# Performance work log

Hardware: AMD Instinct MI355X
Metric: run time of the kernel (lower is better)

## Reference

```python
import jax, jax.numpy as jnp
import numpy as np

N_ROWS = 4096   # output features (N)
M_COLS = 4096   # input features (M)
BATCH = 4096
NNZ_PER_ROW = 819


def setup_inputs() -> dict:
    rng = np.random.default_rng(0)
    # sample NNZ_PER_ROW distinct, sorted column indices per row (CSR structure)
    cols = np.argsort(rng.random((N_ROWS, M_COLS)), axis=1)[:, :NNZ_PER_ROW]
    cols = np.sort(cols, axis=1).reshape(-1).astype(np.int32)            # [nnz]
    row_ids = np.repeat(np.arange(N_ROWS, dtype=np.int32), NNZ_PER_ROW)  # [nnz], expanded indptr

    key = jax.random.key(0)
    k1, k2, k3 = jax.random.split(key, 3)
    inp = jax.random.normal(k1, (BATCH, M_COLS), dtype=jnp.float32)
    W_val = jax.random.normal(k2, (N_ROWS * NNZ_PER_ROW,), dtype=jnp.float32) * 0.02
    bias = jax.random.normal(k3, (N_ROWS,), dtype=jnp.float32)
    return {
        "input": inp,
        "W_val": W_val,
        "bias": bias,
        "row_ids": jnp.asarray(row_ids),
        "cols": jnp.asarray(cols),
        "N": N_ROWS,
    }


def reference(input, W_val, bias, row_ids, cols, N):
    # Faithful math of SparseLinearFunction: y = x @ W^T + bias where W is the
    # CSR matrix (W_val, row_ids, cols) of shape (N, M). Densify via scatter
    # (CSR has unique (row, col) pairs) then use a single GEMM.
    M = input.shape[-1]
    W = jnp.zeros((N, M), dtype=W_val.dtype).at[row_ids, cols].set(W_val)  # [N, M]
    return jnp.matmul(input, W.T) + bias  # [B, N]
```

## Files before the change

### kernel.cpp

```cpp
#include <hip/hip_runtime.h>
#include <hip/hip_bf16.h>
#include <stdint.h>


#define B_DIM 4096
#define M_DIM 4096
#define N_DIM 4096
#define NNZ_ROW 819

typedef __attribute__((ext_vector_type(8))) __bf16 bf16x8;
typedef __attribute__((ext_vector_type(4))) float f32x4;

__device__ __forceinline__ unsigned short f32_to_bf16(float f) {
    union { float f; unsigned int u; } v;
    v.f = f;
    unsigned int r = v.u + 0x7FFFu + ((v.u >> 16) & 1u);
    return (unsigned short)(r >> 16);
}

__device__ __forceinline__ void load_lds16(const void* g, void* l) {
    __builtin_amdgcn_global_load_lds(
        (const __attribute__((address_space(1))) void*)g,
        (__attribute__((address_space(3))) void*)l,
        16, 0, 0);
}

__global__ __launch_bounds__(256) void prep(
    const float* __restrict__ wval,
    const int* __restrict__ cols,
    unsigned short* __restrict__ wb,
    const float4* __restrict__ x,
    uint4* __restrict__ xb) {
    const int tid = threadIdx.x;
    if (blockIdx.x >= N_DIM) {
        const int i = (blockIdx.x - N_DIM) * 256 + tid;
        const float4 a = x[2 * i];
        const float4 b = x[2 * i + 1];
        union { ushort ush[8]; uint4 u4; } o;
        o.ush[0] = f32_to_bf16(a.x); o.ush[1] = f32_to_bf16(a.y);
        o.ush[2] = f32_to_bf16(a.z); o.ush[3] = f32_to_bf16(a.w);
        o.ush[4] = f32_to_bf16(b.x); o.ush[5] = f32_to_bf16(b.y);
        o.ush[6] = f32_to_bf16(b.z); o.ush[7] = f32_to_bf16(b.w);
        xb[i] = o.u4;
        return;
    }
    __shared__ __attribute__((aligned(16))) unsigned short row_s[M_DIM];
    const int row = blockIdx.x;
    uint4* rs4 = (uint4*)row_s;
    rs4[tid]       = make_uint4(0u, 0u, 0u, 0u);
    rs4[tid + 256] = make_uint4(0u, 0u, 0u, 0u);
    __syncthreads();
    const size_t base = (size_t)row * NNZ_ROW;
    for (int j = tid; j < NNZ_ROW; j += 256) {
        const int c = cols[base + j];
        row_s[c] = f32_to_bf16(wval[base + j]);
    }
    __syncthreads();
    uint4* dst = (uint4*)(wb + (size_t)row * M_DIM);
    dst[tid]       = rs4[tid];
    dst[tid + 256] = rs4[tid + 256];
}

__device__ __forceinline__ void stage_half(
    const unsigned short* __restrict__ src,
    int grow0, int kt, unsigned short* dst, int w, int l) {
#pragma unroll
    for (int j = 0; j < 2; ++j) {
        const int seg = w * 2 + j;
        const int r   = seg * 8 + (l >> 3);
        const int cg  = (l >> 3) ^ (l & 7);
        load_lds16(src + (size_t)(grow0 + r) * M_DIM + kt + cg * 8,
                   dst + seg * 512);
    }
}

template <int MA, int KS, bool RDB, int SK, int WAITN>
__device__ __forceinline__ void phase_op(
    const unsigned short* As_c, const unsigned short* Bs_c,
    unsigned short* As_n, unsigned short* Bs_n,
    const unsigned short* __restrict__ Xb, const unsigned short* __restrict__ Wb,
    int bm0, int bn0, int kn, bool do_stage,
    int wr, int wc, int w, int l,
    bf16x8 (&bfr)[2][2], f32x4 (&acc)[2][4][2][2]) {
    const int l15 = l & 15;
    const int lg  = l >> 4;
    const int lx  = l & 7;
    const int ck  = ((KS * 4 + lg) ^ lx) << 3;

    const unsigned short* Ab = As_c + (MA * 128 + wr * 64 + l15) * 64;
    bf16x8 af[4];
#pragma unroll
    for (int mf = 0; mf < 4; ++mf)
        af[mf] = *(const bf16x8*)(Ab + mf * 1024 + ck);

    if constexpr (RDB) {
#pragma unroll
        for (int nb = 0; nb < 2; ++nb) {
            const unsigned short* Bb = Bs_c + (nb * 128 + wc * 32 + l15) * 64;
#pragma unroll
            for (int nf = 0; nf < 2; ++nf)
                bfr[nb][nf] = *(const bf16x8*)(Bb + nf * 1024 + ck);
        }
    }

    if (do_stage) {
        if constexpr (SK == 0) {
            stage_half(Xb, bm0,       kn, As_n,        w, l);
            stage_half(Wb, bn0,       kn, Bs_n,        w, l);
        }
        if constexpr (SK == 1) stage_half(Wb, bn0 + 128, kn, Bs_n + 8192, w, l);
        if constexpr (SK == 2) stage_half(Xb, bm0 + 128, kn, As_n + 8192, w, l);
    }

    if constexpr (WAITN >= 0) __builtin_amdgcn_s_waitcnt(0x0F70 | WAITN);
    __builtin_amdgcn_s_barrier();

    __builtin_amdgcn_s_setprio(1);
#pragma unroll
    for (int mf = 0; mf < 4; ++mf)
#pragma unroll
        for (int nb = 0; nb < 2; ++nb)
#pragma unroll
            for (int nf = 0; nf < 2; ++nf)
                acc[MA][mf][nb][nf] = __builtin_amdgcn_mfma_f32_16x16x32_bf16(
                    af[mf], bfr[nb][nf], acc[MA][mf][nb][nf], 0, 0, 0);
    __builtin_amdgcn_s_setprio(0);
    __builtin_amdgcn_s_barrier();
    __builtin_amdgcn_sched_barrier(0);
}

__global__ __launch_bounds__(512, 2) void gemm_bt_bias(
    const unsigned short* __restrict__ Xb,
    const unsigned short* __restrict__ Wb,
    const float* __restrict__ bias,
    float* __restrict__ out)
{
    __shared__ __attribute__((aligned(16))) unsigned short As0[16384];
    __shared__ __attribute__((aligned(16))) unsigned short Bs0[16384];
    __shared__ __attribute__((aligned(16))) unsigned short As1[16384];
    __shared__ __attribute__((aligned(16))) unsigned short Bs1[16384];

    const int tid = threadIdx.x;
    const int w   = tid >> 6;
    const int l   = tid & 63;
    const int wr  = w >> 2;
    const int wc  = w & 3;

    const int wg  = blockIdx.y * 16 + blockIdx.x;
    const int idx = ((wg & 7) << 5) | (wg >> 3);
    const int bm0 = (idx >> 4) * 256;
    const int bn0 = (idx & 15) * 256;

    f32x4 acc[2][4][2][2];
#pragma unroll
    for (int a = 0; a < 2; ++a)
#pragma unroll
        for (int b = 0; b < 4; ++b)
#pragma unroll
            for (int c = 0; c < 2; ++c)
#pragma unroll
                for (int d = 0; d < 2; ++d) acc[a][b][c][d] = (f32x4)0.0f;

    bf16x8 bfr[2][2];

    stage_half(Xb, bm0,       0, As0,        w, l);
    stage_half(Wb, bn0,       0, Bs0,        w, l);
    stage_half(Xb, bm0 + 128, 0, As0 + 8192, w, l);
    stage_half(Wb, bn0 + 128, 0, Bs0 + 8192, w, l);
    __builtin_amdgcn_s_waitcnt(0x0F70);
    __builtin_amdgcn_s_barrier();

#define TILE4(AC, BC, AN, BN, KN, DS)                                          \
    phase_op<0, 0, true , 0,  4>(AC, BC, AN, BN, Xb, Wb, bm0, bn0, KN, DS,     \
                                 wr, wc, w, l, bfr, acc);                      \
    phase_op<1, 0, false, 1, -1>(AC, BC, AN, BN, Xb, Wb, bm0, bn0, KN, DS,     \
                                 wr, wc, w, l, bfr, acc);                      \
    phase_op<0, 1, true , 2, -1>(AC, BC, AN, BN, Xb, Wb, bm0, bn0, KN, DS,     \
                                 wr, wc, w, l, bfr, acc);                      \
    phase_op<1, 1, false, 3,  2>(AC, BC, AN, BN, Xb, Wb, bm0, bn0, KN, DS,     \
                                 wr, wc, w, l, bfr, acc);

#pragma unroll 1
    for (int kt = 0; kt < M_DIM - 128; kt += 128) {
        const int k1 = kt + 64;
        const int k2 = kt + 128;
        TILE4(As0, Bs0, As1, Bs1, k1, true)
        TILE4(As1, Bs1, As0, Bs0, k2, true)
    }
    TILE4(As0, Bs0, As1, Bs1, M_DIM - 64, true)
    phase_op<0, 0, true , 3,  0>(As1, Bs1, As0, Bs0, Xb, Wb, bm0, bn0, 0, false,
                                 wr, wc, w, l, bfr, acc);
    phase_op<1, 0, false, 3, -1>(As1, Bs1, As0, Bs0, Xb, Wb, bm0, bn0, 0, false,
                                 wr, wc, w, l, bfr, acc);
    phase_op<0, 1, true , 3, -1>(As1, Bs1, As0, Bs0, Xb, Wb, bm0, bn0, 0, false,
                                 wr, wc, w, l, bfr, acc);
    phase_op<1, 1, false, 3, -1>(As1, Bs1, As0, Bs0, Xb, Wb, bm0, bn0, 0, false,
                                 wr, wc, w, l, bfr, acc);
#undef TILE4

    const int l15 = l & 15;
    const int lg  = l >> 4;
#pragma unroll
    for (int nb = 0; nb < 2; ++nb)
#pragma unroll
        for (int nf = 0; nf < 2; ++nf) {
            const int col = bn0 + nb * 128 + wc * 32 + nf * 16 + l15;
            const float bv = bias[col];
#pragma unroll
            for (int ma = 0; ma < 2; ++ma)
#pragma unroll
                for (int mf = 0; mf < 4; ++mf) {
                    const int row0 = bm0 + ma * 128 + wr * 64 + mf * 16 + lg * 4;
#pragma unroll
                    for (int r = 0; r < 4; ++r)
                        out[(size_t)(row0 + r) * N_DIM + col] =
                            acc[ma][mf][nb][nf][r] + bv;
                }
        }
}


extern "C" void kernel_launch(void* const* d_in, const int* in_sizes, int n_in,
                              void* d_out, int out_size, void* d_ws, size_t ws_size,
                              hipStream_t stream) {
    const float* x       = (const float*)d_in[0];
    const float* wval    = (const float*)d_in[1];
    const float* bias    = (const float*)d_in[2];
    const int*   cols    = (const int*)d_in[4];
    float* out = (float*)d_out;

    unsigned short* Wb = (unsigned short*)d_ws;
    unsigned short* Xb = Wb + (size_t)N_DIM * M_DIM;

    prep<<<dim3(N_DIM + (B_DIM * M_DIM) / 8 / 256), dim3(256), 0, stream>>>(
        wval, cols, Wb, (const float4*)x, (uint4*)Xb);
    gemm_bt_bias<<<dim3(N_DIM / 256, B_DIM / 256), dim3(512), 0, stream>>>(
        Xb, Wb, bias, out);
}
```

Before: 280.1 us.

## Restructure GEMM k-loop into one barrier per k-tile with interleaved LDS reads

The four-phase-per-k-tile schedule is replaced by a single ktile routine. It waits for all outstanding global-to-LDS loads and hits one barrier per tile, then issues all four half-tile stages for the next buffer at once. LDS fragment reads for the next MFMA group are interleaved between the MFMA groups, removing the per-phase double barriers and the staggered partial waitcnts. This cuts synchronization overhead but uses more fragment registers and drops the finer-grained overlap of staging with compute.

```diff
diff --git a/kernel.cpp b/kernel.cpp
--- a/kernel.cpp
+++ b/kernel.cpp
@@ -74,59 +74,79 @@
     }
 }
 
-template <int MA, int KS, bool RDB, int SK, int WAITN>
-__device__ __forceinline__ void phase_op(
+#define MFMA_STEP(MA, ASET, BSET)                                              \
+    __builtin_amdgcn_s_setprio(1);                                             \
+    _Pragma("unroll")                                                          \
+    for (int mf = 0; mf < 4; ++mf)                                             \
+        _Pragma("unroll")                                                      \
+        for (int nb = 0; nb < 2; ++nb)                                         \
+            _Pragma("unroll")                                                  \
+            for (int nf = 0; nf < 2; ++nf)                                     \
+                acc[MA][mf][nb][nf] =                                          \
+                    __builtin_amdgcn_mfma_f32_16x16x32_bf16(                   \
+                        ASET[mf], BSET[nb][nf], acc[MA][mf][nb][nf], 0, 0, 0); \
+    __builtin_amdgcn_s_setprio(0);
+
+__device__ __forceinline__ void ktile(
     const unsigned short* As_c, const unsigned short* Bs_c,
     unsigned short* As_n, unsigned short* Bs_n,
     const unsigned short* __restrict__ Xb, const unsigned short* __restrict__ Wb,
-    int bm0, int bn0, int kn, bool do_stage,
-    int wr, int wc, int w, int l,
-    bf16x8 (&bfr)[2][2], f32x4 (&acc)[2][4][2][2]) {
+    int bm0, int bn0, int knext, bool do_stage,
+    int wr, int wc, int w, int l, f32x4 (&acc)[2][4][2][2])
+{
+    __builtin_amdgcn_s_waitcnt(0x0F70);
+    __builtin_amdgcn_s_barrier();
+
     const int l15 = l & 15;
     const int lg  = l >> 4;
     const int lx  = l & 7;
-    const int ck  = ((KS * 4 + lg) ^ lx) << 3;
-
-    const unsigned short* Ab = As_c + (MA * 128 + wr * 64 + l15) * 64;
-    bf16x8 af[4];
-#pragma unroll
-    for (int mf = 0; mf < 4; ++mf)
-        af[mf] = *(const bf16x8*)(Ab + mf * 1024 + ck);
-
-    if constexpr (RDB) {
-#pragma unroll
-        for (int nb = 0; nb < 2; ++nb) {
-            const unsigned short* Bb = Bs_c + (nb * 128 + wc * 32 + l15) * 64;
-#pragma unroll
-            for (int nf = 0; nf < 2; ++nf)
-                bfr[nb][nf] = *(const bf16x8*)(Bb + nf * 1024 + ck);
-        }
-    }
-
+    const int ck0 = (lg ^ lx) << 3;
+    const int ck1 = ((4 + lg) ^ lx) << 3;
+
+    const unsigned short* A0 = As_c + (wr * 64 + l15) * 64;
+    const unsigned short* A1 = A0 + 128 * 64;
+    const unsigned short* B0 = Bs_c + (wc * 32 + l15) * 64;
+    const unsigned short* B1 = B0 + 128 * 64;
+
+    bf16x8 a0k0[4], a1k0[4], a0k1[4], a1k1[4], bk0[2][2], bk1[2][2];
+
+#pragma unroll
+    for (int mf = 0; mf < 4; ++mf)
+        a0k0[mf] = *(const bf16x8*)(A0 + mf * 1024 + ck0);
+#pragma unroll
+    for (int nf = 0; nf < 2; ++nf) {
+        bk0[0][nf] = *(const bf16x8*)(B0 + nf * 1024 + ck0);
+        bk0[1][nf] = *(const bf16x8*)(B1 + nf * 1024 + ck0);
+    }
     if (do_stage) {
-        if constexpr (SK == 0) {
-            stage_half(Xb, bm0,       kn, As_n,        w, l);
-            stage_half(Wb, bn0,       kn, Bs_n,        w, l);
-        }
-        if constexpr (SK == 1) stage_half(Wb, bn0 + 128, kn, Bs_n + 8192, w, l);
-        if constexpr (SK == 2) stage_half(Xb, bm0 + 128, kn, As_n + 8192, w, l);
-    }
-
-    if constexpr (WAITN >= 0) __builtin_amdgcn_s_waitcnt(0x0F70 | WAITN);
-    __builtin_amdgcn_s_barrier();
-
-    __builtin_amdgcn_s_setprio(1);
-#pragma unroll
-    for (int mf = 0; mf < 4; ++mf)
-#pragma unroll
-        for (int nb = 0; nb < 2; ++nb)
-#pragma unroll
-            for (int nf = 0; nf < 2; ++nf)
-                acc[MA][mf][nb][nf] = __builtin_amdgcn_mfma_f32_16x16x32_bf16(
-                    af[mf], bfr[nb][nf], acc[MA][mf][nb][nf], 0, 0, 0);
-    __builtin_amdgcn_s_setprio(0);
-    __builtin_amdgcn_s_barrier();
-    __builtin_amdgcn_sched_barrier(0);
+        stage_half(Xb, bm0,       knext, As_n,        w, l);
+        stage_half(Wb, bn0,       knext, Bs_n,        w, l);
+        stage_half(Xb, bm0 + 128, knext, As_n + 8192, w, l);
+        stage_half(Wb, bn0 + 128, knext, Bs_n + 8192, w, l);
+    }
+#pragma unroll
+    for (int mf = 0; mf < 4; ++mf)
+        a1k0[mf] = *(const bf16x8*)(A1 + mf * 1024 + ck0);
+
+    MFMA_STEP(0, a0k0, bk0)
+
+#pragma unroll
+    for (int mf = 0; mf < 4; ++mf)
+        a0k1[mf] = *(const bf16x8*)(A0 + mf * 1024 + ck1);
+#pragma unroll
+    for (int nf = 0; nf < 2; ++nf) {
+        bk1[0][nf] = *(const bf16x8*)(B0 + nf * 1024 + ck1);
+        bk1[1][nf] = *(const bf16x8*)(B1 + nf * 1024 + ck1);
+    }
+
+    MFMA_STEP(1, a1k0, bk0)
+
+#pragma unroll
+    for (int mf = 0; mf < 4; ++mf)
+        a1k1[mf] = *(const bf16x8*)(A1 + mf * 1024 + ck1);
+
+    MFMA_STEP(0, a0k1, bk1)
+    MFMA_STEP(1, a1k1, bk1)
 }
 
 __global__ __launch_bounds__(512, 2) void gemm_bt_bias(
@@ -161,42 +181,18 @@
 #pragma unroll
                 for (int d = 0; d < 2; ++d) acc[a][b][c][d] = (f32x4)0.0f;
 
-    bf16x8 bfr[2][2];
-
     stage_half(Xb, bm0,       0, As0,        w, l);
     stage_half(Wb, bn0,       0, Bs0,        w, l);
     stage_half(Xb, bm0 + 128, 0, As0 + 8192, w, l);
     stage_half(Wb, bn0 + 128, 0, Bs0 + 8192, w, l);
-    __builtin_amdgcn_s_waitcnt(0x0F70);
-    __builtin_amdgcn_s_barrier();
-
-#define TILE4(AC, BC, AN, BN, KN, DS)                                          \
-    phase_op<0, 0, true , 0,  4>(AC, BC, AN, BN, Xb, Wb, bm0, bn0, KN, DS,     \
-                                 wr, wc, w, l, bfr, acc);                      \
-    phase_op<1, 0, false, 1, -1>(AC, BC, AN, BN, Xb, Wb, bm0, bn0, KN, DS,     \
-                                 wr, wc, w, l, bfr, acc);                      \
-    phase_op<0, 1, true , 2, -1>(AC, BC, AN, BN, Xb, Wb, bm0, bn0, KN, DS,     \
-                                 wr, wc, w, l, bfr, acc);                      \
-    phase_op<1, 1, false, 3,  2>(AC, BC, AN, BN, Xb, Wb, bm0, bn0, KN, DS,     \
-                                 wr, wc, w, l, bfr, acc);
 
 #pragma unroll 1
-    for (int kt = 0; kt < M_DIM - 128; kt += 128) {
-        const int k1 = kt + 64;
-        const int k2 = kt + 128;
-        TILE4(As0, Bs0, As1, Bs1, k1, true)
-        TILE4(As1, Bs1, As0, Bs0, k2, true)
-    }
-    TILE4(As0, Bs0, As1, Bs1, M_DIM - 64, true)
-    phase_op<0, 0, true , 3,  0>(As1, Bs1, As0, Bs0, Xb, Wb, bm0, bn0, 0, false,
-                                 wr, wc, w, l, bfr, acc);
-    phase_op<1, 0, false, 3, -1>(As1, Bs1, As0, Bs0, Xb, Wb, bm0, bn0, 0, false,
-                                 wr, wc, w, l, bfr, acc);
-    phase_op<0, 1, true , 3, -1>(As1, Bs1, As0, Bs0, Xb, Wb, bm0, bn0, 0, false,
-                                 wr, wc, w, l, bfr, acc);
-    phase_op<1, 1, false, 3, -1>(As1, Bs1, As0, Bs0, Xb, Wb, bm0, bn0, 0, false,
-                                 wr, wc, w, l, bfr, acc);
-#undef TILE4
+    for (int kt = 0; kt < M_DIM; kt += 128) {
+        ktile(As0, Bs0, As1, Bs1, Xb, Wb, bm0, bn0, kt + 64, true,
+              wr, wc, w, l, acc);
+        ktile(As1, Bs1, As0, Bs0, Xb, Wb, bm0, bn0, kt + 128,
+              kt + 128 < M_DIM, wr, wc, w, l, acc);
+    }
 
     const int l15 = l & 15;
     const int lg  = l >> 4;
```

After: 329.8 us. 1.18x slower.

## Remap warp tiles to contiguous 128x64 and simplify staging waits

Applied to the files above, without the earlier changes.

Each warp now owns a contiguous 128-row by 64-column output block instead of split 2x2 sub-blocks, so B fragments are read as four contiguous 16-column slices. Staging is reordered so both A halves load first and the B halves follow. The per-phase partial waitcnt is replaced by one full wait at the last phase, the peeled tail is folded into the loop with a conditional stage, and the sched_barrier is removed. The change may alter LDS bank patterns and reduces how much load latency overlaps with compute, since every tile now ends in a full drain.

```diff
diff --git a/kernel.cpp b/kernel.cpp
--- a/kernel.cpp
+++ b/kernel.cpp
@@ -74,59 +74,53 @@
     }
 }
 
-template <int MA, int KS, bool RDB, int SK, int WAITN>
+template <int MA, int KS, bool RDB, int SK>
 __device__ __forceinline__ void phase_op(
     const unsigned short* As_c, const unsigned short* Bs_c,
     unsigned short* As_n, unsigned short* Bs_n,
     const unsigned short* __restrict__ Xb, const unsigned short* __restrict__ Wb,
     int bm0, int bn0, int kn, bool do_stage,
-    int wr, int wc, int w, int l,
-    bf16x8 (&bfr)[2][2], f32x4 (&acc)[2][4][2][2]) {
+    int wm, int wn, int w, int l,
+    bf16x8 (&bfr)[4], f32x4 (&acc)[2][4][4]) {
     const int l15 = l & 15;
     const int lg  = l >> 4;
     const int lx  = l & 7;
     const int ck  = ((KS * 4 + lg) ^ lx) << 3;
 
-    const unsigned short* Ab = As_c + (MA * 128 + wr * 64 + l15) * 64;
+    const unsigned short* Ab = As_c + (wm * 128 + MA * 64 + l15) * 64;
     bf16x8 af[4];
 #pragma unroll
     for (int mf = 0; mf < 4; ++mf)
         af[mf] = *(const bf16x8*)(Ab + mf * 1024 + ck);
 
     if constexpr (RDB) {
-#pragma unroll
-        for (int nb = 0; nb < 2; ++nb) {
-            const unsigned short* Bb = Bs_c + (nb * 128 + wc * 32 + l15) * 64;
-#pragma unroll
-            for (int nf = 0; nf < 2; ++nf)
-                bfr[nb][nf] = *(const bf16x8*)(Bb + nf * 1024 + ck);
-        }
+        const unsigned short* Bb = Bs_c + (wn * 64 + l15) * 64;
+#pragma unroll
+        for (int nf = 0; nf < 4; ++nf)
+            bfr[nf] = *(const bf16x8*)(Bb + nf * 1024 + ck);
     }
 
     if (do_stage) {
         if constexpr (SK == 0) {
             stage_half(Xb, bm0,       kn, As_n,        w, l);
-            stage_half(Wb, bn0,       kn, Bs_n,        w, l);
+            stage_half(Xb, bm0 + 128, kn, As_n + 8192, w, l);
         }
-        if constexpr (SK == 1) stage_half(Wb, bn0 + 128, kn, Bs_n + 8192, w, l);
-        if constexpr (SK == 2) stage_half(Xb, bm0 + 128, kn, As_n + 8192, w, l);
-    }
-
-    if constexpr (WAITN >= 0) __builtin_amdgcn_s_waitcnt(0x0F70 | WAITN);
+        if constexpr (SK == 1) stage_half(Wb, bn0,       kn, Bs_n,        w, l);
+        if constexpr (SK == 2) stage_half(Wb, bn0 + 128, kn, Bs_n + 8192, w, l);
+    }
+    if constexpr (SK == 3)
+        __builtin_amdgcn_s_waitcnt(0x0F70);
     __builtin_amdgcn_s_barrier();
 
     __builtin_amdgcn_s_setprio(1);
 #pragma unroll
     for (int mf = 0; mf < 4; ++mf)
 #pragma unroll
-        for (int nb = 0; nb < 2; ++nb)
-#pragma unroll
-            for (int nf = 0; nf < 2; ++nf)
-                acc[MA][mf][nb][nf] = __builtin_amdgcn_mfma_f32_16x16x32_bf16(
-                    af[mf], bfr[nb][nf], acc[MA][mf][nb][nf], 0, 0, 0);
+        for (int nf = 0; nf < 4; ++nf)
+            acc[MA][mf][nf] = __builtin_amdgcn_mfma_f32_16x16x32_bf16(
+                af[mf], bfr[nf], acc[MA][mf][nf], 0, 0, 0);
     __builtin_amdgcn_s_setprio(0);
     __builtin_amdgcn_s_barrier();
-    __builtin_amdgcn_sched_barrier(0);
 }
 
 __global__ __launch_bounds__(512, 2) void gemm_bt_bias(
@@ -143,80 +137,65 @@
     const int tid = threadIdx.x;
     const int w   = tid >> 6;
     const int l   = tid & 63;
-    const int wr  = w >> 2;
-    const int wc  = w & 3;
+    const int wm  = w >> 2;
+    const int wn  = w & 3;
 
     const int wg  = blockIdx.y * 16 + blockIdx.x;
     const int idx = ((wg & 7) << 5) | (wg >> 3);
     const int bm0 = (idx >> 4) * 256;
     const int bn0 = (idx & 15) * 256;
 
-    f32x4 acc[2][4][2][2];
+    f32x4 acc[2][4][4];
 #pragma unroll
     for (int a = 0; a < 2; ++a)
 #pragma unroll
         for (int b = 0; b < 4; ++b)
 #pragma unroll
-            for (int c = 0; c < 2; ++c)
-#pragma unroll
-                for (int d = 0; d < 2; ++d) acc[a][b][c][d] = (f32x4)0.0f;
-
-    bf16x8 bfr[2][2];
+            for (int c = 0; c < 4; ++c) acc[a][b][c] = (f32x4)0.0f;
+
+    bf16x8 bfr[4];
 
     stage_half(Xb, bm0,       0, As0,        w, l);
+    stage_half(Xb, bm0 + 128, 0, As0 + 8192, w, l);
     stage_half(Wb, bn0,       0, Bs0,        w, l);
-    stage_half(Xb, bm0 + 128, 0, As0 + 8192, w, l);
     stage_half(Wb, bn0 + 128, 0, Bs0 + 8192, w, l);
     __builtin_amdgcn_s_waitcnt(0x0F70);
     __builtin_amdgcn_s_barrier();
 
 #define TILE4(AC, BC, AN, BN, KN, DS)                                          \
-    phase_op<0, 0, true , 0,  4>(AC, BC, AN, BN, Xb, Wb, bm0, bn0, KN, DS,     \
-                                 wr, wc, w, l, bfr, acc);                      \
-    phase_op<1, 0, false, 1, -1>(AC, BC, AN, BN, Xb, Wb, bm0, bn0, KN, DS,     \
-                                 wr, wc, w, l, bfr, acc);                      \
-    phase_op<0, 1, true , 2, -1>(AC, BC, AN, BN, Xb, Wb, bm0, bn0, KN, DS,     \
-                                 wr, wc, w, l, bfr, acc);                      \
-    phase_op<1, 1, false, 3,  2>(AC, BC, AN, BN, Xb, Wb, bm0, bn0, KN, DS,     \
-                                 wr, wc, w, l, bfr, acc);
+    phase_op<0, 0, true , 0>(AC, BC, AN, BN, Xb, Wb, bm0, bn0, KN, DS,         \
+                             wm, wn, w, l, bfr, acc);                          \
+    phase_op<1, 0, false, 1>(AC, BC, AN, BN, Xb, Wb, bm0, bn0, KN, DS,         \
+                             wm, wn, w, l, bfr, acc);                          \
+    phase_op<0, 1, true , 2>(AC, BC, AN, BN, Xb, Wb, bm0, bn0, KN, DS,         \
+                             wm, wn, w, l, bfr, acc);                          \
+    phase_op<1, 1, false, 3>(AC, BC, AN, BN, Xb, Wb, bm0, bn0, KN, DS,         \
+                             wm, wn, w, l, bfr, acc);
 
 #pragma unroll 1
-    for (int kt = 0; kt < M_DIM - 128; kt += 128) {
-        const int k1 = kt + 64;
-        const int k2 = kt + 128;
-        TILE4(As0, Bs0, As1, Bs1, k1, true)
-        TILE4(As1, Bs1, As0, Bs0, k2, true)
-    }
-    TILE4(As0, Bs0, As1, Bs1, M_DIM - 64, true)
-    phase_op<0, 0, true , 3,  0>(As1, Bs1, As0, Bs0, Xb, Wb, bm0, bn0, 0, false,
-                                 wr, wc, w, l, bfr, acc);
-    phase_op<1, 0, false, 3, -1>(As1, Bs1, As0, Bs0, Xb, Wb, bm0, bn0, 0, false,
-                                 wr, wc, w, l, bfr, acc);
-    phase_op<0, 1, true , 3, -1>(As1, Bs1, As0, Bs0, Xb, Wb, bm0, bn0, 0, false,
-                                 wr, wc, w, l, bfr, acc);
-    phase_op<1, 1, false, 3, -1>(As1, Bs1, As0, Bs0, Xb, Wb, bm0, bn0, 0, false,
-                                 wr, wc, w, l, bfr, acc);
+    for (int kt = 0; kt < M_DIM; kt += 128) {
+        TILE4(As0, Bs0, As1, Bs1, kt + 64, true)
+        TILE4(As1, Bs1, As0, Bs0, kt + 128, kt + 128 < M_DIM)
+    }
 #undef TILE4
 
     const int l15 = l & 15;
     const int lg  = l >> 4;
 #pragma unroll
-    for (int nb = 0; nb < 2; ++nb)
-#pragma unroll
-        for (int nf = 0; nf < 2; ++nf) {
-            const int col = bn0 + nb * 128 + wc * 32 + nf * 16 + l15;
-            const float bv = bias[col];
-#pragma unroll
-            for (int ma = 0; ma < 2; ++ma)
-#pragma unroll
-                for (int mf = 0; mf < 4; ++mf) {
-                    const int row0 = bm0 + ma * 128 + wr * 64 + mf * 16 + lg * 4;
-#pragma unroll
-                    for (int r = 0; r < 4; ++r)
-                        out[(size_t)(row0 + r) * N_DIM + col] =
-                            acc[ma][mf][nb][nf][r] + bv;
-                }
-        }
+    for (int nf = 0; nf < 4; ++nf) {
+        const int col = bn0 + wn * 64 + nf * 16 + l15;
+        const float bv = bias[col];
+#pragma unroll
+        for (int ma = 0; ma < 2; ++ma)
+#pragma unroll
+            for (int mf = 0; mf < 4; ++mf) {
+                const int row0 = bm0 + wm * 128 + ma * 64 + mf * 16 + lg * 4;
+#pragma unroll
+                for (int r = 0; r < 4; ++r)
+                    out[(size_t)(row0 + r) * N_DIM + col] =
+                        acc[ma][mf][nf][r] + bv;
+            }
+    }
 }
 
 
```

Result: faster. 262.1 us (-6.4%).
